# Performance work log

Hardware: AMD Instinct MI355X
Metric: run time of the kernel (lower is better)

## Reference

```python
import jax, jax.numpy as jnp
import numpy as np

N = 50000      # nodes
E = 500000     # edges
D = 128        # model dim (in_dim == out_dim)
H = 8          # heads
DH = D // H    # head dim = 16
BN_EPS = 1e-5
Z_EPS = 1e-6


def setup_inputs() -> dict:
    key = jax.random.key(0)
    ks = jax.random.split(key, 24)
    w = lambda k, shape, s=0.05: (jax.random.normal(k, shape, jnp.float32) * s)
    inp = {}
    inp['v'] = jax.random.normal(ks[0], (N, D), jnp.float32)
    inp['e'] = jax.random.normal(ks[1], (E, D), jnp.float32)
    inp['envelope'] = jax.random.uniform(ks[2], (E, 1, 1), jnp.float32)
    inp['src'] = jax.random.randint(ks[3], (E,), 0, N, jnp.int32)
    inp['dst'] = jax.random.randint(ks[4], (E,), 0, N, jnp.int32)
    # attention projections (use_bias=False)
    inp['WQ'] = w(ks[5], (D, D)); inp['WK'] = w(ks[6], (D, D))
    inp['WV'] = w(ks[7], (D, D)); inp['We'] = w(ks[8], (D, D))
    # output projections
    inp['WO_v'] = w(ks[9], (D, D)); inp['bO_v'] = jnp.zeros((D,), jnp.float32)
    inp['WO_e'] = w(ks[10], (D, D)); inp['bO_e'] = jnp.zeros((D,), jnp.float32)
    # batch-norm affine params
    inp['g1_v'] = jnp.ones((D,), jnp.float32); inp['b1_v'] = jnp.zeros((D,), jnp.float32)
    inp['g1_e'] = jnp.ones((D,), jnp.float32); inp['b1_e'] = jnp.zeros((D,), jnp.float32)
    inp['g2_v'] = jnp.ones((D,), jnp.float32); inp['b2_v'] = jnp.zeros((D,), jnp.float32)
    inp['g2_e'] = jnp.ones((D,), jnp.float32); inp['b2_e'] = jnp.zeros((D,), jnp.float32)
    # FFN weights (hidden = 2*D)
    inp['W1v'] = w(ks[11], (D, 2 * D)); inp['b1v'] = jnp.zeros((2 * D,), jnp.float32)
    inp['W2v'] = w(ks[12], (2 * D, D)); inp['b2v'] = jnp.zeros((D,), jnp.float32)
    inp['W1e'] = w(ks[13], (D, 2 * D)); inp['b1e'] = jnp.zeros((2 * D,), jnp.float32)
    inp['W2e'] = w(ks[14], (2 * D, D)); inp['b2e'] = jnp.zeros((D,), jnp.float32)
    return inp


def _batchnorm(x, g, b):
    # BatchNorm1d in training mode: biased batch stats over axis 0
    m = x.mean(0)
    var = x.var(0)
    return (x - m) * jax.lax.rsqrt(var + BN_EPS) * g + b


def _forward(v, e, envelope, src, dst,
             WQ, WK, WV, We, WO_v, bO_v, WO_e, bO_e,
             g1_v, b1_v, g1_e, b1_e,
             W1v, b1v, W2v, b2v, W1e, b1e, W2e, b2e,
             g2_v, b2_v, g2_e, b2_e):
    # --- multi-head edge attention ---
    Q = (v @ WQ).reshape(N, H, DH)
    K = (v @ WK).reshape(N, H, DH)
    V = (v @ WV).reshape(N, H, DH)
    pe = (e @ We).reshape(E, H, DH)
    # score = K[src] * Q[dst] / sqrt(Dh) * proj_e   (elementwise, per head)
    score = K[src] * Q[dst] / np.sqrt(DH).astype(np.float32) * pe  # [E,H,Dh]
    e_attn = score.reshape(E, D)                                    # e_out
    s = jnp.exp(jnp.clip(score.sum(-1, keepdims=True), -5.0, 5.0))  # [E,H,1]
    msg = V[src] * envelope * s                                     # [E,H,Dh]
    wV = jax.ops.segment_sum(msg, dst, num_segments=N)              # [N,H,Dh]
    z = jax.ops.segment_sum(s, dst, num_segments=N)                 # [N,H,1]
    v_attn = (wV / (z + Z_EPS)).reshape(N, D)
    # --- O projection + residual + batchnorm ---
    v1 = _batchnorm(v + (v_attn @ WO_v + bO_v), g1_v, b1_v)
    e1 = _batchnorm(e + (e_attn @ WO_e + bO_e), g1_e, b1_e)
    # --- FFN + residual + batchnorm ---
    v2 = _batchnorm(v1 + (jax.nn.relu(v1 @ W1v + b1v) @ W2v + b2v), g2_v, b2_v)
    e2 = _batchnorm(e1 + (jax.nn.relu(e1 @ W1e + b1e) @ W2e + b2e), g2_e, b2_e)
    return v2, e2


def reference(v, e, envelope, src, dst,
              WQ, WK, WV, We, WO_v, bO_v, WO_e, bO_e,
              g1_v, b1_v, g1_e, b1_e,
              W1v, b1v, W2v, b2v, W1e, b1e, W2e, b2e,
              g2_v, b2_v, g2_e, b2_e):
    return _forward(v, e, envelope, src, dst,
                    WQ, WK, WV, We, WO_v, bO_v, WO_e, bO_e,
                    g1_v, b1_v, g1_e, b1_e,
                    W1v, b1v, W2v, b2v, W1e, b1e, W2e, b2e,
                    g2_v, b2_v, g2_e, b2_e)
```

## Files before the change

kernel.cpp:

```cpp
#include <hip/hip_runtime.h>
#include <hip/hip_bf16.h>

#define N_NODES 50000
#define N_EDGES 500000
#define DIM 128
#define RSTRIDE 256

typedef __bf16 bf16_t;
typedef __bf16 bf16x8 __attribute__((ext_vector_type(8)));
typedef __bf16 bf16x2 __attribute__((ext_vector_type(2)));
typedef float f32x4 __attribute__((ext_vector_type(4)));

#define MFMA(a,b,c) __builtin_amdgcn_mfma_f32_16x16x32_bf16((a),(b),(c),0,0,0)

__device__ __forceinline__ int swz(int row, int kbyte){ return kbyte ^ ((row & 7) << 4); }
__device__ __forceinline__ int hswz(int row, int kbyte){ return kbyte ^ ((row & 15) << 4); }

__device__ __forceinline__ bf16x8 lds_frag(const char* s, int row, int rowb, int kbyte){
  return *(const bf16x8*)(s + row * rowb + swz(row, kbyte));
}

__device__ __forceinline__ void copy16(char* dst, const char* __restrict__ src, int bytes){
  for (int o = threadIdx.x * 16; o < bytes; o += blockDim.x * 16)
    *(f32x4*)(dst + o) = *(const f32x4*)(src + o);
}

struct WPrep {
  const float* w[10];
  int Kd[10], Nd[10], off[10], cum[10], mode[10];
};

__global__ void k_wprep(WPrep d, char* img, int total){
  for (int idx = blockIdx.x * blockDim.x + threadIdx.x; idx < total; idx += gridDim.x * blockDim.x){
    int i = 0;
#pragma unroll
    for (int j = 1; j < 10; j++) if (idx >= d.cum[j]) i = j;
    int loc = idx - d.cum[i];
    int K = d.Kd[i], N = d.Nd[i];
    int n = loc / K, k = loc - n * K;
    float val = d.w[i][(size_t)k * N + n];
    int nn = n;
    if (d.mode[i] == 1) nn = ((n & 7) << 4) | (n >> 3);
    if (d.mode[i] == 3) nn = ((n & 15) << 4) | (n >> 4);
    *(bf16_t*)(img + d.off[i] + nn * (K * 2) + swz(nn, k * 2)) = (bf16_t)val;
  }
}

__global__ void k_count(const int* __restrict__ dst, int* __restrict__ cnt){
  int i = blockIdx.x * blockDim.x + threadIdx.x;
  if (i < N_EDGES) atomicAdd(&cnt[dst[i]], 1);
}

__global__ __launch_bounds__(1024) void k_scan(const int* __restrict__ cnt,
                                               int* __restrict__ rowptr, int* __restrict__ wp){
  __shared__ int wsum[16];
  __shared__ int wpre[16];
  __shared__ int scarry;
  const int tid = threadIdx.x, lane = tid & 63, wv = tid >> 6;
  if (tid == 0) scarry = 0;
  for (int base = 0; base < N_NODES; base += 8192){
    int i0 = base + tid * 8;
    int v[8], p[8];
    int tsum = 0;
#pragma unroll
    for (int j = 0; j < 8; j++){
      int idx = i0 + j;
      v[j] = (idx < N_NODES) ? cnt[idx] : 0;
      p[j] = tsum; tsum += v[j];
    }
    int x = tsum;
#pragma unroll
    for (int off = 1; off < 64; off <<= 1){
      int t = __shfl_up(x, off);
      if (lane >= off) x += t;
    }
    if (lane == 63) wsum[wv] = x;
    __syncthreads();
    if (tid == 0){
      int run = scarry;
#pragma unroll
      for (int j = 0; j < 16; j++){ int t = wsum[j]; wpre[j] = run; run += t; }
      scarry = run;
    }
    __syncthreads();
    int texcl = wpre[wv] + x - tsum;
#pragma unroll
    for (int j = 0; j < 8; j++){
      int idx = i0 + j;
      if (idx < N_NODES){ rowptr[idx] = texcl + p[j]; wp[idx] = texcl + p[j]; }
    }
  }
  __syncthreads();
  if (tid == 0) rowptr[N_NODES] = scarry;
}

__global__ void k_fill(const int* __restrict__ dst, int* __restrict__ wp, int* __restrict__ csr){
  int i = blockIdx.x * blockDim.x + threadIdx.x;
  if (i < N_EDGES){
    int p = atomicAdd(&wp[dst[i]], 1);
    csr[p] = i;
  }
}

__global__ __launch_bounds__(512) void k_qkv(
    const float* __restrict__ v, const char* __restrict__ img,
    bf16_t* __restrict__ Q, bf16_t* __restrict__ K, bf16_t* __restrict__ V, int M)
{
  __shared__ __align__(16) char sm[65536];
  char* sX = sm;
  char* sW = sm + 32768;
  const int tid = threadIdx.x, lane = tid & 63, wave = tid >> 6;
  const int r0 = blockIdx.x * 128;
  for (int c = tid; c < 2048; c += 512){
    int row = c >> 4, kc = c & 15, grow = r0 + row;
    float f[8];
    if (grow < M){
      const float4* p = (const float4*)(v + (size_t)grow * DIM + kc * 8);
      float4 u0 = p[0], u1 = p[1];
      f[0]=u0.x; f[1]=u0.y; f[2]=u0.z; f[3]=u0.w;
      f[4]=u1.x; f[5]=u1.y; f[6]=u1.z; f[7]=u1.w;
    } else {
#pragma unroll
      for (int j=0;j<8;j++) f[j] = 0.f;
    }
    bf16x8 o;
#pragma unroll
    for (int j=0;j<8;j++) o[j] = (bf16_t)f[j];
    *(bf16x8*)(sX + row * 256 + swz(row, kc * 16)) = o;
  }
  const int rowA = wave * 16 + (lane & 15);
  const int kb0 = (lane >> 4) * 16;
  const int crow = wave*16 + (lane >> 4)*4;
  const int ccol = lane & 15;
  const f32x4 zero4 = {0.f, 0.f, 0.f, 0.f};
#pragma unroll
  for (int w3 = 0; w3 < 3; w3++){
    __syncthreads();
    copy16(sW, img + w3 * 32768, 32768);
    __syncthreads();
    f32x4 acc[8];
#pragma unroll
    for (int b=0;b<8;b++) acc[b] = zero4;
#pragma unroll
    for (int ks=0; ks<4; ks++){
      bf16x8 a = lds_frag(sX, rowA, 256, ks*64 + kb0);
#pragma unroll
      for (int nt=0; nt<8; nt++){
        int rn = nt*16 + (lane & 15);
        bf16x8 b = lds_frag(sW, rn, 256, ks*64 + kb0);
        acc[nt] = MFMA(a, b, acc[nt]);
      }
    }
    bf16_t* o = (w3 == 0) ? Q : ((w3 == 1) ? K : V);
#pragma unroll
    for (int r=0; r<4; r++){
      int grow = r0 + crow + r;
      if (grow < M){
        bf16x8 t;
#pragma unroll
        for (int nt=0; nt<8; nt++) t[nt] = (bf16_t)acc[nt][r];
        *(bf16x8*)(o + (size_t)grow * DIM + ccol*8) = t;
      }
    }
  }
}

__global__ __launch_bounds__(512, 4) void k_edge(
    const float* __restrict__ e,
    const int* __restrict__ src, const int* __restrict__ dst,
    const bf16_t* __restrict__ Qb, const bf16_t* __restrict__ Kb,
    const char* __restrict__ imgWe, const char* __restrict__ imgWo,
    const float* __restrict__ bOe,
    bf16_t* __restrict__ e1_pre, float* __restrict__ sv,
    float* __restrict__ stats, int M)
{
  __shared__ __align__(16) char sm[66560];
  char* sW = sm;
  char* sX = sm + 32768;
  float* sStats = (float*)(sm + 65536);
  const int tid = threadIdx.x, lane = tid & 63, wave = tid >> 6;
  const int r0 = blockIdx.x * 128;
  const int crow = wave*16 + (lane >> 4)*4;
  const int ccol = lane & 15;
  const int rowA = wave * 16 + (lane & 15);
  const int q = lane >> 4;
  const int kb0 = q * 16;
  bf16x8 Kg[4], Qg[4];
#pragma unroll
  for (int r=0;r<4;r++){
    int ed = r0 + crow + r; if (ed >= M) ed = M - 1;
    int sn = src[ed], dn = dst[ed];
    Kg[r] = *(const bf16x8*)(Kb + (size_t)sn * DIM + ccol * 8);
    Qg[r] = *(const bf16x8*)(Qb + (size_t)dn * DIM + ccol * 8);
  }
  int grA = r0 + rowA; if (grA >= M) grA = M - 1;
  const f32x4* epA = (const f32x4*)(e + (size_t)grA * DIM);
  f32x4 ea[8];
#pragma unroll
  for (int ks=0; ks<4; ks++){
    ea[2*ks]   = epA[ks*8 + q*2];
    ea[2*ks+1] = epA[ks*8 + q*2 + 1];
  }
  copy16(sW, imgWe, 32768);
  if (tid < 256) sStats[tid] = 0.f;
  bf16x8 eAb[4];
#pragma unroll
  for (int ks=0; ks<4; ks++){
#pragma unroll
    for (int j=0;j<4;j++){
      eAb[ks][j]   = (bf16_t)ea[2*ks][j];
      eAb[ks][4+j] = (bf16_t)ea[2*ks+1][j];
    }
  }
  __syncthreads();
  const f32x4 zero4 = {0.f,0.f,0.f,0.f};
  f32x4 wbuf[4];
#pragma unroll
  for (int i=0;i<4;i++) wbuf[i] = *(const f32x4*)(imgWo + tid*16 + i*8192);
  f32x4 pe[8];
#pragma unroll
  for (int i=0;i<8;i++) pe[i] = zero4;
#pragma unroll
  for (int ks=0; ks<4; ks++){
#pragma unroll
    for (int nt=0; nt<8; nt++){
      int rn = nt*16 + (lane & 15);
      bf16x8 b = lds_frag(sW, rn, 256, ks*64 + kb0);
      pe[nt] = MFMA(eAb[ks], b, pe[nt]);
    }
  }
  __syncthreads();
#pragma unroll
  for (int i=0;i<4;i++) *(f32x4*)(sW + tid*16 + i*8192) = wbuf[i];
  f32x4 er[8];
#pragma unroll
  for (int r=0;r<4;r++){
    int gr = r0 + crow + r; if (gr >= M) gr = M - 1;
    const f32x4* rp = (const f32x4*)(e + (size_t)gr*DIM + ccol*8);
    er[2*r]   = rp[0];
    er[2*r+1] = rp[1];
  }
#pragma unroll
  for (int r=0;r<4;r++){
    int row = crow + r;
    bf16x8 t;
    float hsum = 0.f;
#pragma unroll
    for (int nt=0; nt<8; nt++){
      float sc = pe[nt][r] * 0.25f * (float)Kg[r][nt] * (float)Qg[r][nt];
      t[nt] = (bf16_t)sc;
      hsum += sc;
    }
    *(bf16x8*)(sX + row*256 + swz(row, ccol*16)) = t;
    float ts = hsum + __shfl_xor(hsum, 1);
    int ed = r0 + row;
    if (!(ccol & 1) && ed < M)
      sv[(size_t)ed*8 + (ccol >> 1)] = __expf(fminf(5.f, fmaxf(-5.f, ts)));
  }
  __syncthreads();
  f32x4 a2[8];
#pragma unroll
  for (int i=0;i<8;i++) a2[i] = zero4;
#pragma unroll
  for (int ks=0; ks<4; ks++){
    bf16x8 a = lds_frag(sX, rowA, 256, ks*64 + kb0);
#pragma unroll
    for (int nt=0; nt<8; nt++){
      int rn = nt*16 + (lane & 15);
      bf16x8 b = lds_frag(sW, rn, 256, ks*64 + kb0);
      a2[nt] = MFMA(a, b, a2[nt]);
    }
  }
  float4 bo0 = *(const float4*)(bOe + ccol*8);
  float4 bo1 = *(const float4*)(bOe + ccol*8 + 4);
  float s1[8], s2[8];
#pragma unroll
  for (int j=0;j<8;j++){ s1[j]=0.f; s2[j]=0.f; }
#pragma unroll
  for (int r=0; r<4; r++){
    int ed = r0 + crow + r;
    float val[8];
    if (ed < M){
      val[0]=a2[0][r]+er[2*r][0]+bo0.x; val[1]=a2[1][r]+er[2*r][1]+bo0.y;
      val[2]=a2[2][r]+er[2*r][2]+bo0.z; val[3]=a2[3][r]+er[2*r][3]+bo0.w;
      val[4]=a2[4][r]+er[2*r+1][0]+bo1.x; val[5]=a2[5][r]+er[2*r+1][1]+bo1.y;
      val[6]=a2[6][r]+er[2*r+1][2]+bo1.z; val[7]=a2[7][r]+er[2*r+1][3]+bo1.w;
      bf16x8 t;
#pragma unroll
      for (int j=0;j<8;j++) t[j] = (bf16_t)val[j];
      *(bf16x8*)(e1_pre + (size_t)ed*RSTRIDE + ccol*8) = t;
    } else {
#pragma unroll
      for (int j=0;j<8;j++) val[j]=0.f;
    }
#pragma unroll
    for (int j=0;j<8;j++){ s1[j] += val[j]; s2[j] += val[j]*val[j]; }
  }
#pragma unroll
  for (int j=0;j<8;j++){
    s1[j] += __shfl_xor(s1[j], 16); s1[j] += __shfl_xor(s1[j], 32);
    s2[j] += __shfl_xor(s2[j], 16); s2[j] += __shfl_xor(s2[j], 32);
  }
  if (lane < 16){
#pragma unroll
    for (int j=0;j<8;j++){
      atomicAdd(&sStats[ccol*8 + j], s1[j]);
      atomicAdd(&sStats[128 + ccol*8 + j], s2[j]);
    }
  }
  __syncthreads();
  if (tid < 256) unsafeAtomicAdd(&stats[tid], sStats[tid]);
}

__global__ __launch_bounds__(512) void k_agg(
    const int* __restrict__ rowptr, const int* __restrict__ csr,
    const int* __restrict__ src, const float* __restrict__ envl,
    const float* __restrict__ sv, const bf16_t* __restrict__ V,
    bf16_t* __restrict__ vAttn, int M)
{
  const int wave = threadIdx.x >> 6, lane = threadIdx.x & 63;
  const int n = blockIdx.x * 8 + wave;
  if (n >= M) return;
  const int beg = rowptr[n], end = rowptr[n + 1];
  const int h = lane >> 3;
  float ax = 0.f, ay = 0.f, zacc = 0.f;
  int i = beg;
  for (; i + 4 <= end; i += 4){
    int e0 = csr[i], e1 = csr[i+1], e2 = csr[i+2], e3 = csr[i+3];
    int sn0 = src[e0], sn1 = src[e1], sn2 = src[e2], sn3 = src[e3];
    float sv0 = sv[(size_t)e0*8 + h], sv1 = sv[(size_t)e1*8 + h];
    float sv2 = sv[(size_t)e2*8 + h], sv3 = sv[(size_t)e3*8 + h];
    float n0 = envl[e0], n1 = envl[e1], n2 = envl[e2], n3 = envl[e3];
    bf16x2 a0 = *(const bf16x2*)(V + (size_t)sn0 * DIM + lane * 2);
    bf16x2 a1 = *(const bf16x2*)(V + (size_t)sn1 * DIM + lane * 2);
    bf16x2 a2v = *(const bf16x2*)(V + (size_t)sn2 * DIM + lane * 2);
    bf16x2 a3 = *(const bf16x2*)(V + (size_t)sn3 * DIM + lane * 2);
    float w0 = n0*sv0, w1 = n1*sv1, w2 = n2*sv2, w3 = n3*sv3;
    ax += (float)a0[0]*w0 + (float)a1[0]*w1 + (float)a2v[0]*w2 + (float)a3[0]*w3;
    ay += (float)a0[1]*w0 + (float)a1[1]*w1 + (float)a2v[1]*w2 + (float)a3[1]*w3;
    zacc += sv0 + sv1 + sv2 + sv3;
// ... 69 lines not shown
      const float4* vp = (const float4*)(v + (size_t)grow*DIM + ccol*8);
      float4 v0 = vp[0], v1 = vp[1];
      val[0]=acc[0][r]+v0.x+bo0.x; val[1]=acc[1][r]+v0.y+bo0.y;
      val[2]=acc[2][r]+v0.z+bo0.z; val[3]=acc[3][r]+v0.w+bo0.w;
      val[4]=acc[4][r]+v1.x+bo1.x; val[5]=acc[5][r]+v1.y+bo1.y;
      val[6]=acc[6][r]+v1.z+bo1.z; val[7]=acc[7][r]+v1.w+bo1.w;
      bf16x8 t;
#pragma unroll
      for (int j=0;j<8;j++) t[j] = (bf16_t)val[j];
      *(bf16x8*)(v1_pre + (size_t)grow*RSTRIDE + ccol*8) = t;
    } else {
#pragma unroll
      for (int j=0;j<8;j++) val[j]=0.f;
    }
#pragma unroll
    for (int j=0;j<8;j++){ s1[j] += val[j]; s2[j] += val[j]*val[j]; }
  }
#pragma unroll
  for (int j=0;j<8;j++){
    s1[j] += __shfl_xor(s1[j], 16); s1[j] += __shfl_xor(s1[j], 32);
    s2[j] += __shfl_xor(s2[j], 16); s2[j] += __shfl_xor(s2[j], 32);
  }
  if (lane < 16){
#pragma unroll
    for (int j=0;j<8;j++){
      atomicAdd(&sStats[ccol*8 + j], s1[j]);
      atomicAdd(&sStats[128 + ccol*8 + j], s2[j]);
    }
  }
  __syncthreads();
  if (tid < 256) unsafeAtomicAdd(&stats[tid], sStats[tid]);
}

__global__ __launch_bounds__(512, 4) void k_ffn(
    bf16_t* __restrict__ xio, const float* __restrict__ ss1,
    const char* __restrict__ img1, const float* __restrict__ b1,
    const char* __restrict__ img2, const float* __restrict__ b2,
    float* __restrict__ stats2, int M)
{
  __shared__ __align__(16) char sm[66560];
  char* sA = sm;
  char* sB = sm + 32768;
  float* sStats = (float*)(sm + 65536);
  const int tid = threadIdx.x, lane = tid & 63, wave = tid >> 6;
  const int r0 = blockIdx.x * 128;
  const int rowA = wave*16 + (lane & 15);
  const int q = lane >> 4;
  const int kb0 = q * 16;
  const int crow = wave*16 + q*4;
  const int ccol = lane & 15;
  const f32x4 zero4 = {0.f,0.f,0.f,0.f};

  float4 sc0 = *(const float4*)(ss1 + ccol*8);
  float4 sc1 = *(const float4*)(ss1 + ccol*8 + 4);
  float4 sh0 = *(const float4*)(ss1 + 128 + ccol*8);
  float4 sh1 = *(const float4*)(ss1 + 128 + ccol*8 + 4);
  const float4* bq = (const float4*)(b1 + ccol * 16);
  float4 bq0 = bq[0], bq1 = bq[1], bq2 = bq[2], bq3 = bq[3];

  copy16(sB, img1, 32768);
  if (tid < 256) sStats[tid] = 0.f;
  int grA = r0 + rowA; if (grA >= M) grA = M - 1;
  const bf16_t* xrow = xio + (size_t)grA * RSTRIDE;
  bf16x8 araw[4];
#pragma unroll
  for (int ks=0; ks<4; ks++)
// ... 88 lines not shown
      t[6]=(bf16_t)fmaxf(acc[6][r]+bq3.z,0.f); t[7]=(bf16_t)fmaxf(acc[7][r]+bq3.w,0.f);
      hreg[4+r] = t;
    }
  }
  __syncthreads();

  f32x4 o2[8];
#pragma unroll
  for (int i=0;i<8;i++) o2[i]=zero4;

#pragma unroll
  for (int half = 0; half < 2; half++){
    if ((ccol >> 3) == half){
      int cb = (ccol & 7) * 32;
#pragma unroll
      for (int r=0;r<4;r++){
        int row = crow + r;
        *(bf16x8*)(sA + row*256 + hswz(row, cb))      = hreg[r];
        *(bf16x8*)(sA + row*256 + hswz(row, cb + 16)) = hreg[4+r];
      }
    }
#pragma unroll
    for (int i=0;i<4;i++) *(f32x4*)(sB + tid*16 + i*8192) = wbuf[i];
    __syncthreads();
    if (half == 0){
#pragma unroll
      for (int i=0;i<4;i++){
        int o = tid*16 + i*8192;
        wbuf[i] = *(const f32x4*)(img2 + (o >> 8)*512 + 256 + (o & 255));
      }
    }
#pragma unroll
    for (int ks=0;ks<4;ks++){
      const char* ap = sA + rowA*256 + hswz(rowA, ks*64+kb0);
      bf16x8 a = *(const bf16x8*)ap;
#pragma unroll
      for (int nt=0;nt<8;nt++){
        int rn = nt*16 + (lane&15);
        bf16x8 b = lds_frag(sB, rn, 256, ks*64+kb0);
        o2[nt] = MFMA(a,b,o2[nt]);
      }
    }
    __syncthreads();
  }

  float4 b20 = *(const float4*)(b2 + ccol*8);
  float4 b21 = *(const float4*)(b2 + ccol*8 + 4);
  float s1[8], s2[8];
#pragma unroll
  for (int j=0;j<8;j++){ s1[j]=0.f; s2[j]=0.f; }
#pragma unroll
  for (int r=0;r<4;r++){
    int grow = r0 + crow + r;
    float val[8];
    val[0]=(float)xres[r][0]+o2[0][r]+b20.x; val[1]=(float)xres[r][1]+o2[1][r]+b20.y;
    val[2]=(float)xres[r][2]+o2[2][r]+b20.z; val[3]=(float)xres[r][3]+o2[3][r]+b20.w;
    val[4]=(float)xres[r][4]+o2[4][r]+b21.x; val[5]=(float)xres[r][5]+o2[5][r]+b21.y;
    val[6]=(float)xres[r][6]+o2[6][r]+b21.z; val[7]=(float)xres[r][7]+o2[7][r]+b21.w;
    if (grow < M){
      bf16x8 t;
#pragma unroll
      for (int j=0;j<8;j++) t[j] = (bf16_t)val[j];
      *(bf16x8*)(xio + (size_t)grow*RSTRIDE + ccol*8) = t;
    } else {
#pragma unroll
      for (int j=0;j<8;j++) val[j]=0.f;
    }
#pragma unroll
    for (int j=0;j<8;j++){ s1[j] += val[j]; s2[j] += val[j]*val[j]; }
  }
#pragma unroll
  for (int j=0;j<8;j++){
    s1[j] += __shfl_xor(s1[j], 16); s1[j] += __shfl_xor(s1[j], 32);
    s2[j] += __shfl_xor(s2[j], 16); s2[j] += __shfl_xor(s2[j], 32);
  }
  if (lane < 16){
#pragma unroll
    for (int j=0;j<8;j++){
      atomicAdd(&sStats[ccol*8 + j], s1[j]);
      atomicAdd(&sStats[128 + ccol*8 + j], s2[j]);
    }
  }
  __syncthreads();
  if (tid < 256) unsafeAtomicAdd(&stats2[tid], sStats[tid]);
}

struct FinArgs { const float* st; const float* g; const float* b; float* ss; float invM; };

__global__ void k_finstats(FinArgs a0, FinArgs a1){
  FinArgs a = (blockIdx.x == 0) ? a0 : a1;
  int c = threadIdx.x;
  float mean = a.st[c] * a.invM;
  float var  = a.st[128 + c] * a.invM - mean * mean;
  float scl  = a.g[c] * rsqrtf(var + 1e-5f);
  a.ss[c] = scl;
  a.ss[128 + c] = a.b[c] - mean * scl;
}

__global__ __launch_bounds__(256) void k_norm2(
    char* __restrict__ xv, char* __restrict__ xe,
    const float* __restrict__ ssv, const float* __restrict__ sse,
    long long nv, long long ne)
{
  long long tv = nv * 16, total = tv + ne * 16;
  for (long long g = (long long)blockIdx.x * blockDim.x + threadIdx.x; g < total;
       g += (long long)gridDim.x * blockDim.x){
    bool isv = g < tv;
    char* base = isv ? xv : xe;
    const float* ss = isv ? ssv : sse;
    long long gg = isv ? g : g - tv;
    long long row = gg >> 4;
    int c = (int)(gg & 15);
    bf16x8 u = *(const bf16x8*)(base + row * 512 + c * 16);
    int c0 = c * 8;
    float4 o0, o1;
    o0.x = (float)u[0]*ss[c0+0] + ss[128+c0+0];
    o0.y = (float)u[1]*ss[c0+1] + ss[128+c0+1];
    o0.z = (float)u[2]*ss[c0+2] + ss[128+c0+2];
    o0.w = (float)u[3]*ss[c0+3] + ss[128+c0+3];
    o1.x = (float)u[4]*ss[c0+4] + ss[128+c0+4];
    o1.y = (float)u[5]*ss[c0+5] + ss[128+c0+5];
    o1.z = (float)u[6]*ss[c0+6] + ss[128+c0+6];
    o1.w = (float)u[7]*ss[c0+7] + ss[128+c0+7];
    float4* dp = (float4*)(base + row * 512 + c * 32);
    dp[0] = o0; dp[1] = o1;
  }
}

extern "C" void kernel_launch(void* const* d_in, const int* in_sizes, int n_in,
                              void* d_out, int out_size, void* d_ws, size_t ws_size,
                              hipStream_t stream)
{
  const float* v    = (const float*)d_in[0];
  const float* e    = (const float*)d_in[1];
  const float* envl = (const float*)d_in[2];
  const int*   src  = (const int*)d_in[3];
  const int*   dst  = (const int*)d_in[4];
  const float* bOv  = (const float*)d_in[10];
  const float* bOe  = (const float*)d_in[12];
  const float* g1v  = (const float*)d_in[13];
  const float* b1vn = (const float*)d_in[14];
  const float* g1e  = (const float*)d_in[15];
// ... 11 lines not shown
  float* out_e = out_v + (size_t)N_NODES * DIM;
  bf16_t* v1b = (bf16_t*)out_v;
  bf16_t* e1b = (bf16_t*)out_e;

  char* ws = (char*)d_ws;
  const size_t IMG_OFF = 0;
  const size_t QB_OFF  = 458752;
  const size_t KB_OFF  = QB_OFF  + 12800000;
  const size_t VB_OFF  = KB_OFF  + 12800000;
  const size_t VA_OFF  = VB_OFF  + 12800000;
  const size_t SV_OFF  = VA_OFF  + 12800000;
  const size_t CSR_OFF = SV_OFF  + 16000000;
  const size_t RP_OFF  = CSR_OFF + 2000000;
  const size_t WP_OFF  = RP_OFF  + 200016;
  const size_t CNT_OFF = WP_OFF  + 200000;
  const size_t ST_OFF  = CNT_OFF + 200000;
  const size_t SS_OFF  = ST_OFF  + 4096;

  char*   img   = ws + IMG_OFF;
  bf16_t* Qb    = (bf16_t*)(ws + QB_OFF);
  bf16_t* Kb    = (bf16_t*)(ws + KB_OFF);
  bf16_t* Vb    = (bf16_t*)(ws + VB_OFF);
  bf16_t* vAttn = (bf16_t*)(ws + VA_OFF);
  float*  svp   = (float*)(ws + SV_OFF);
  int*    csr   = (int*)(ws + CSR_OFF);
  int*    rowp  = (int*)(ws + RP_OFF);
  int*    wpp   = (int*)(ws + WP_OFF);
  int*    cnt   = (int*)(ws + CNT_OFF);
  float*  st    = (float*)(ws + ST_OFF);
  float*  ssb   = (float*)(ws + SS_OFF);
  float* st_e1 = st;        float* st_v1 = st + 256;
  float* st_v2 = st + 512;  float* st_e2 = st + 768;
  float* ss_v1 = ssb;       float* ss_e1 = ssb + 256;
  float* ss_v2 = ssb + 512; float* ss_e2 = ssb + 768;

  (void)hipMemsetAsync(ws + CNT_OFF, 0, 200000 + 4096, stream);

  WPrep wp;
  const int wid[10]   = {5,6,7,8,9,11,21,23,25,27};
  const int Ks[10]    = {128,128,128,128,128,128,128,256,128,256};
  const int Ns[10]    = {128,128,128,128,128,128,256,128,256,128};
  const int modes[10] = {1,1,1,1,1,1,3,1,3,1};
  int cum = 0, off = 0;
  for (int i = 0; i < 10; i++){
    wp.w[i] = (const float*)d_in[wid[i]];
    wp.Kd[i] = Ks[i]; wp.Nd[i] = Ns[i];
    wp.off[i] = off; wp.cum[i] = cum; wp.mode[i] = modes[i];
    off += Ks[i]*Ns[i]*2; cum += Ks[i]*Ns[i];
  }
  k_wprep<<<896, 256, 0, stream>>>(wp, img, cum);

  k_count<<<1954, 256, 0, stream>>>(dst, cnt);
  k_scan<<<1, 1024, 0, stream>>>(cnt, rowp, wpp);
  k_fill<<<1954, 256, 0, stream>>>(dst, wpp, csr);

  k_qkv<<<391, 512, 0, stream>>>(v, img, Qb, Kb, Vb, N_NODES);

  k_edge<<<3907, 512, 0, stream>>>(e, src, dst, Qb, Kb,
                                   img + 98304 , img + 163840 , bOe,
                                   e1b, svp, st_e1, N_EDGES);

  k_agg<<<6250, 512, 0, stream>>>(rowp, csr, src, envl, svp, Vb, vAttn, N_NODES);

  k_nodeout<<<391, 512, 0, stream>>>(vAttn, v, img + 131072 , bOv,
                                     v1b, st_v1, N_NODES);

  {
    FinArgs fv{st_v1, g1v, b1vn, ss_v1, 1.f / N_NODES};
    FinArgs fe{st_e1, g1e, b1en, ss_e1, 1.f / N_EDGES};
    k_finstats<<<2, 128, 0, stream>>>(fv, fe);
  }

  k_ffn<<<391, 512, 0, stream>>>(v1b, ss_v1, img + 196608 , b1vf,
                                 img + 262144 , b2vf, st_v2, N_NODES);
  k_ffn<<<3907, 512, 0, stream>>>(e1b, ss_e1, img + 327680 , b1ef,
                                  img + 393216 , b2ef, st_e2, N_EDGES);

  {
    FinArgs fv{st_v2, g2v, b2vn, ss_v2, 1.f / N_NODES};
    FinArgs fe{st_e2, g2e, b2en, ss_e2, 1.f / N_EDGES};
    k_finstats<<<2, 128, 0, stream>>>(fv, fe);
  }

  k_norm2<<<4096, 256, 0, stream>>>((char*)out_v, (char*)out_e, ss_v2, ss_e2,
                                    (long long)N_NODES, (long long)N_EDGES);
}
```

Baseline: 723.9 us.

## Fuse CSR build kernels into weight-prep, QKV and edge kernels; fold finstats into norm

Merges the weight-prep and degree-count kernels into one launch, runs the prefix scan as an extra block alongside the QKV GEMM, and appends the CSR fill as extra blocks of the edge kernel. The final BN stats finalize is computed per block inside the normalization kernel, which removes one more launch. The goal is fewer kernel launches and letting the small serial stages overlap with bigger work. In exchange, the single scan block now has 512 threads and may become the tail of the QKV launch, and every norm block recomputes the scale and shift.

```diff
diff --git a/kernel.cpp b/kernel.cpp
--- a/kernel.cpp
+++ b/kernel.cpp
@@ -30,151 +30,151 @@
   int Kd[10], Nd[10], off[10], cum[10], mode[10];
 };
 
-__global__ void k_wprep(WPrep d, char* img, int total){
-  for (int idx = blockIdx.x * blockDim.x + threadIdx.x; idx < total; idx += gridDim.x * blockDim.x){
-    int i = 0;
-#pragma unroll
-    for (int j = 1; j < 10; j++) if (idx >= d.cum[j]) i = j;
-    int loc = idx - d.cum[i];
-    int K = d.Kd[i], N = d.Nd[i];
-    int n = loc / K, k = loc - n * K;
-    float val = d.w[i][(size_t)k * N + n];
-    int nn = n;
-    if (d.mode[i] == 1) nn = ((n & 7) << 4) | (n >> 3);
-    if (d.mode[i] == 3) nn = ((n & 15) << 4) | (n >> 4);
-    *(bf16_t*)(img + d.off[i] + nn * (K * 2) + swz(nn, k * 2)) = (bf16_t)val;
-  }
-}
-
-__global__ void k_count(const int* __restrict__ dst, int* __restrict__ cnt){
-  int i = blockIdx.x * blockDim.x + threadIdx.x;
-  if (i < N_EDGES) atomicAdd(&cnt[dst[i]], 1);
-}
-
-__global__ __launch_bounds__(1024) void k_scan(const int* __restrict__ cnt,
-                                               int* __restrict__ rowptr, int* __restrict__ wp){
-  __shared__ int wsum[16];
-  __shared__ int wpre[16];
-  __shared__ int scarry;
-  const int tid = threadIdx.x, lane = tid & 63, wv = tid >> 6;
-  if (tid == 0) scarry = 0;
-  for (int base = 0; base < N_NODES; base += 8192){
-    int i0 = base + tid * 8;
-    int v[8], p[8];
-    int tsum = 0;
-#pragma unroll
-    for (int j = 0; j < 8; j++){
-      int idx = i0 + j;
-      v[j] = (idx < N_NODES) ? cnt[idx] : 0;
-      p[j] = tsum; tsum += v[j];
-    }
-    int x = tsum;
-#pragma unroll
-    for (int off = 1; off < 64; off <<= 1){
-      int t = __shfl_up(x, off);
-      if (lane >= off) x += t;
-    }
-    if (lane == 63) wsum[wv] = x;
-    __syncthreads();
-    if (tid == 0){
-      int run = scarry;
-#pragma unroll
-      for (int j = 0; j < 16; j++){ int t = wsum[j]; wpre[j] = run; run += t; }
-      scarry = run;
-    }
-    __syncthreads();
-    int texcl = wpre[wv] + x - tsum;
-#pragma unroll
-    for (int j = 0; j < 8; j++){
-      int idx = i0 + j;
-      if (idx < N_NODES){ rowptr[idx] = texcl + p[j]; wp[idx] = texcl + p[j]; }
-    }
-  }
-  __syncthreads();
-  if (tid == 0) rowptr[N_NODES] = scarry;
-}
-
-__global__ void k_fill(const int* __restrict__ dst, int* __restrict__ wp, int* __restrict__ csr){
-  int i = blockIdx.x * blockDim.x + threadIdx.x;
-  if (i < N_EDGES){
-    int p = atomicAdd(&wp[dst[i]], 1);
-    csr[p] = i;
-  }
-}
-
-__global__ __launch_bounds__(512) void k_qkv(
+__global__ __launch_bounds__(512) void k_prep(WPrep d, char* img,
+                                              const int* __restrict__ dst, int* __restrict__ cnt){
+  if (blockIdx.x < 448){
+    int idx = blockIdx.x * 512 + threadIdx.x;
+    if (idx < 229376){
+      int i = 0;
+#pragma unroll
+      for (int j = 1; j < 10; j++) if (idx >= d.cum[j]) i = j;
+      int loc = idx - d.cum[i];
+      int K = d.Kd[i], N = d.Nd[i];
+      int n = loc / K, k = loc - n * K;
+      float val = d.w[i][(size_t)k * N + n];
+      int nn = n;
+      if (d.mode[i] == 1) nn = ((n & 7) << 4) | (n >> 3);
+      if (d.mode[i] == 3) nn = ((n & 15) << 4) | (n >> 4);
+      *(bf16_t*)(img + d.off[i] + nn * (K * 2) + swz(nn, k * 2)) = (bf16_t)val;
+    }
+  } else {
+    int i = (blockIdx.x - 448) * 512 + threadIdx.x;
+    if (i < N_EDGES) atomicAdd(&cnt[dst[i]], 1);
+  }
+}
+
+__global__ __launch_bounds__(512) void k_qkv_scan(
     const float* __restrict__ v, const char* __restrict__ img,
-    bf16_t* __restrict__ Q, bf16_t* __restrict__ K, bf16_t* __restrict__ V, int M)
+    bf16_t* __restrict__ Q, bf16_t* __restrict__ K, bf16_t* __restrict__ V, int M,
+    const int* __restrict__ cnt, int* __restrict__ rowptr, int* __restrict__ wp)
 {
   __shared__ __align__(16) char sm[65536];
-  char* sX = sm;
-  char* sW = sm + 32768;
+  __shared__ int wsum[8], wpre[8], scarry_s;
   const int tid = threadIdx.x, lane = tid & 63, wave = tid >> 6;
-  const int r0 = blockIdx.x * 128;
-  for (int c = tid; c < 2048; c += 512){
-    int row = c >> 4, kc = c & 15, grow = r0 + row;
-    float f[8];
-    if (grow < M){
-      const float4* p = (const float4*)(v + (size_t)grow * DIM + kc * 8);
-      float4 u0 = p[0], u1 = p[1];
-      f[0]=u0.x; f[1]=u0.y; f[2]=u0.z; f[3]=u0.w;
-      f[4]=u1.x; f[5]=u1.y; f[6]=u1.z; f[7]=u1.w;
-    } else {
-#pragma unroll
-      for (int j=0;j<8;j++) f[j] = 0.f;
-    }
-    bf16x8 o;
-#pragma unroll
-    for (int j=0;j<8;j++) o[j] = (bf16_t)f[j];
-    *(bf16x8*)(sX + row * 256 + swz(row, kc * 16)) = o;
-  }
-  const int rowA = wave * 16 + (lane & 15);
-  const int kb0 = (lane >> 4) * 16;
-  const int crow = wave*16 + (lane >> 4)*4;
-  const int ccol = lane & 15;
-  const f32x4 zero4 = {0.f, 0.f, 0.f, 0.f};
-#pragma unroll
-  for (int w3 = 0; w3 < 3; w3++){
-    __syncthreads();
-    copy16(sW, img + w3 * 32768, 32768);
-    __syncthreads();
-    f32x4 acc[8];
-#pragma unroll
-    for (int b=0;b<8;b++) acc[b] = zero4;
-#pragma unroll
-    for (int ks=0; ks<4; ks++){
-      bf16x8 a = lds_frag(sX, rowA, 256, ks*64 + kb0);
-#pragma unroll
-      for (int nt=0; nt<8; nt++){
-        int rn = nt*16 + (lane & 15);
-        bf16x8 b = lds_frag(sW, rn, 256, ks*64 + kb0);
-        acc[nt] = MFMA(a, b, acc[nt]);
-      }
-    }
-    bf16_t* o = (w3 == 0) ? Q : ((w3 == 1) ? K : V);
-#pragma unroll
-    for (int r=0; r<4; r++){
-      int grow = r0 + crow + r;
+  if (blockIdx.x < 391){
+    char* sX = sm;
+    char* sW = sm + 32768;
+    const int r0 = blockIdx.x * 128;
+    for (int c = tid; c < 2048; c += 512){
+      int row = c >> 4, kc = c & 15, grow = r0 + row;
+      float f[8];
       if (grow < M){
-        bf16x8 t;
-#pragma unroll
-        for (int nt=0; nt<8; nt++) t[nt] = (bf16_t)acc[nt][r];
-        *(bf16x8*)(o + (size_t)grow * DIM + ccol*8) = t;
-      }
-    }
-  }
-}
-
-__global__ __launch_bounds__(512, 4) void k_edge(
+        const float4* p = (const float4*)(v + (size_t)grow * DIM + kc * 8);
+        float4 u0 = p[0], u1 = p[1];
+        f[0]=u0.x; f[1]=u0.y; f[2]=u0.z; f[3]=u0.w;
+        f[4]=u1.x; f[5]=u1.y; f[6]=u1.z; f[7]=u1.w;
+      } else {
+#pragma unroll
+        for (int j=0;j<8;j++) f[j] = 0.f;
+      }
+      bf16x8 o;
+#pragma unroll
+      for (int j=0;j<8;j++) o[j] = (bf16_t)f[j];
+      *(bf16x8*)(sX + row * 256 + swz(row, kc * 16)) = o;
+    }
+    const int rowA = wave * 16 + (lane & 15);
+    const int kb0 = (lane >> 4) * 16;
+    const int crow = wave*16 + (lane >> 4)*4;
+    const int ccol = lane & 15;
+    const f32x4 zero4 = {0.f, 0.f, 0.f, 0.f};
+#pragma unroll
+    for (int w3 = 0; w3 < 3; w3++){
+      __syncthreads();
+      copy16(sW, img + w3 * 32768, 32768);
+      __syncthreads();
+      f32x4 acc[8];
+#pragma unroll
+      for (int b=0;b<8;b++) acc[b] = zero4;
+#pragma unroll
+      for (int ks=0; ks<4; ks++){
+        bf16x8 a = lds_frag(sX, rowA, 256, ks*64 + kb0);
+#pragma unroll
+        for (int nt=0; nt<8; nt++){
+          int rn = nt*16 + (lane & 15);
+          bf16x8 b = lds_frag(sW, rn, 256, ks*64 + kb0);
+          acc[nt] = MFMA(a, b, acc[nt]);
+        }
+      }
+      bf16_t* o = (w3 == 0) ? Q : ((w3 == 1) ? K : V);
+#pragma unroll
+      for (int r=0; r<4; r++){
+        int grow = r0 + crow + r;
+        if (grow < M){
+          bf16x8 t;
+#pragma unroll
+          for (int nt=0; nt<8; nt++) t[nt] = (bf16_t)acc[nt][r];
+          *(bf16x8*)(o + (size_t)grow * DIM + ccol*8) = t;
+        }
+      }
+    }
+  } else {
+    if (tid == 0) scarry_s = 0;
+    for (int base = 0; base < N_NODES; base += 4096){
+      int i0 = base + tid * 8;
+      int vv[8], pp[8];
+      int tsum = 0;
+#pragma unroll
+      for (int j = 0; j < 8; j++){
+        int idx = i0 + j;
+        vv[j] = (idx < N_NODES) ? cnt[idx] : 0;
+        pp[j] = tsum; tsum += vv[j];
+      }
+      int x = tsum;
+#pragma unroll
+      for (int off = 1; off < 64; off <<= 1){
+        int t = __shfl_up(x, off);
+        if (lane >= off) x += t;
+      }
+      if (lane == 63) wsum[wave] = x;
+      __syncthreads();
+      if (tid == 0){
+        int run = scarry_s;
+#pragma unroll
+        for (int j = 0; j < 8; j++){ int t = wsum[j]; wpre[j] = run; run += t; }
+        scarry_s = run;
+      }
+      __syncthreads();
+      int texcl = wpre[wave] + x - tsum;
+#pragma unroll
+      for (int j = 0; j < 8; j++){
+        int idx = i0 + j;
+        if (idx < N_NODES){ rowptr[idx] = texcl + pp[j]; wp[idx] = texcl + pp[j]; }
+      }
+      __syncthreads();
+    }
+    if (tid == 0) rowptr[N_NODES] = scarry_s;
+  }
+}
+
+__global__ __launch_bounds__(512, 4) void k_edge_fill(
     const float* __restrict__ e,
     const int* __restrict__ src, const int* __restrict__ dst,
     const bf16_t* __restrict__ Qb, const bf16_t* __restrict__ Kb,
     const char* __restrict__ imgWe, const char* __restrict__ imgWo,
     const float* __restrict__ bOe,
     bf16_t* __restrict__ e1_pre, float* __restrict__ sv,
-    float* __restrict__ stats, int M)
+    float* __restrict__ stats, int M,
+    int* __restrict__ wpF, int* __restrict__ csrF)
 {
   __shared__ __align__(16) char sm[66560];
+  if (blockIdx.x >= 3907){
+    int i = (blockIdx.x - 3907) * 512 + threadIdx.x;
+    if (i < N_EDGES){
+      int pp = atomicAdd(&wpF[dst[i]], 1);
+      csrF[pp] = i;
+    }
+    return;
+  }
   char* sW = sm;
   char* sX = sm + 32768;
   float* sStats = (float*)(sm + 65536);
@@ -441,6 +441,18 @@
   if (tid < 256) unsafeAtomicAdd(&stats[tid], sStats[tid]);
 }
 
+struct FinArgs { const float* st; const float* g; const float* b; float* ss; float invM; };
+
+__global__ void k_finstats(FinArgs a0, FinArgs a1){
+  FinArgs a = (blockIdx.x == 0) ? a0 : a1;
+  int c = threadIdx.x;
+  float mean = a.st[c] * a.invM;
+  float var  = a.st[128 + c] * a.invM - mean * mean;
+  float scl  = a.g[c] * rsqrtf(var + 1e-5f);
+  a.ss[c] = scl;
+  a.ss[128 + c] = a.b[c] - mean * scl;
+}
+
 __global__ __launch_bounds__(512, 4) void k_ffn(
     bf16_t* __restrict__ xio, const float* __restrict__ ss1,
     const char* __restrict__ img1, const float* __restrict__ b1,
@@ -595,8 +607,7 @@
     }
 #pragma unroll
     for (int ks=0;ks<4;ks++){
-      const char* ap = sA + rowA*256 + hswz(rowA, ks*64+kb0);
-      bf16x8 a = *(const bf16x8*)ap;
+      bf16x8 a = *(const bf16x8*)(sA + rowA*256 + hswz(rowA, ks*64+kb0));
 #pragma unroll
       for (int nt=0;nt<8;nt++){
         int rn = nt*16 + (lane&15);
@@ -648,29 +659,30 @@
   if (tid < 256) unsafeAtomicAdd(&stats2[tid], sStats[tid]);
 }
 
-struct FinArgs { const float* st; const float* g; const float* b; float* ss; float invM; };
-
-__global__ void k_finstats(FinArgs a0, FinArgs a1){
-  FinArgs a = (blockIdx.x == 0) ? a0 : a1;
-  int c = threadIdx.x;
-  float mean = a.st[c] * a.invM;
-  float var  = a.st[128 + c] * a.invM - mean * mean;
-  float scl  = a.g[c] * rsqrtf(var + 1e-5f);
-  a.ss[c] = scl;
-  a.ss[128 + c] = a.b[c] - mean * scl;
-}
+struct NormP { const float* st; const float* g; const float* bn; float invM; };
 
 __global__ __launch_bounds__(256) void k_norm2(
     char* __restrict__ xv, char* __restrict__ xe,
-    const float* __restrict__ ssv, const float* __restrict__ sse,
-    long long nv, long long ne)
+    NormP pv, NormP pe, long long nv, long long ne)
 {
+  __shared__ float sSS[512];
+  const int tid = threadIdx.x;
+  {
+    int side = tid >> 7, c = tid & 127;
+    NormP pp = side ? pe : pv;
+    float mean = pp.st[c] * pp.invM;
+    float var  = pp.st[128 + c] * pp.invM - mean * mean;
+    float scl  = pp.g[c] * rsqrtf(var + 1e-5f);
+    sSS[side*256 + c] = scl;
+    sSS[side*256 + 128 + c] = pp.bn[c] - mean * scl;
+  }
+  __syncthreads();
   long long tv = nv * 16, total = tv + ne * 16;
-  for (long long g = (long long)blockIdx.x * blockDim.x + threadIdx.x; g < total;
+  for (long long g = (long long)blockIdx.x * blockDim.x + tid; g < total;
        g += (long long)gridDim.x * blockDim.x){
     bool isv = g < tv;
     char* base = isv ? xv : xe;
-    const float* ss = isv ? ssv : sse;
+    const float* ss = isv ? sSS : (sSS + 256);
     long long gg = isv ? g : g - tv;
     long long row = gg >> 4;
     int c = (int)(gg & 15);
@@ -748,7 +760,6 @@
   float* st_e1 = st;        float* st_v1 = st + 256;
   float* st_v2 = st + 512;  float* st_e2 = st + 768;
   float* ss_v1 = ssb;       float* ss_e1 = ssb + 256;
-  float* ss_v2 = ssb + 512; float* ss_e2 = ssb + 768;
 
   (void)hipMemsetAsync(ws + CNT_OFF, 0, 200000 + 4096, stream);
 
@@ -764,40 +775,26 @@
     wp.off[i] = off; wp.cum[i] = cum; wp.mode[i] = modes[i];
     off += Ks[i]*Ns[i]*2; cum += Ks[i]*Ns[i];
   }
-  k_wprep<<<896, 256, 0, stream>>>(wp, img, cum);
-
-  k_count<<<1954, 256, 0, stream>>>(dst, cnt);
-  k_scan<<<1, 1024, 0, stream>>>(cnt, rowp, wpp);
-  k_fill<<<1954, 256, 0, stream>>>(dst, wpp, csr);
-
-  k_qkv<<<391, 512, 0, stream>>>(v, img, Qb, Kb, Vb, N_NODES);
-
-  k_edge<<<3907, 512, 0, stream>>>(e, src, dst, Qb, Kb,
-                                   img + 98304 , img + 163840 , bOe,
-                                   e1b, svp, st_e1, N_EDGES);
-
+
+  k_prep<<<1425, 512, 0, stream>>>(wp, img, dst, cnt);
+  k_qkv_scan<<<392, 512, 0, stream>>>(v, img, Qb, Kb, Vb, N_NODES, cnt, rowp, wpp);
+  k_edge_fill<<<4884, 512, 0, stream>>>(e, src, dst, Qb, Kb,
+                                        img + 98304 , img + 163840 , bOe,
+                                        e1b, svp, st_e1, N_EDGES, wpp, csr);
   k_agg<<<6250, 512, 0, stream>>>(rowp, csr, src, envl, svp, Vb, vAttn, N_NODES);
-
   k_nodeout<<<391, 512, 0, stream>>>(vAttn, v, img + 131072 , bOv,
                                      v1b, st_v1, N_NODES);
-
   {
     FinArgs fv{st_v1, g1v, b1vn, ss_v1, 1.f / N_NODES};
     FinArgs fe{st_e1, g1e, b1en, ss_e1, 1.f / N_EDGES};
     k_finstats<<<2, 128, 0, stream>>>(fv, fe);
   }
-
   k_ffn<<<391, 512, 0, stream>>>(v1b, ss_v1, img + 196608 , b1vf,
                                  img + 262144 , b2vf, st_v2, N_NODES);
   k_ffn<<<3907, 512, 0, stream>>>(e1b, ss_e1, img + 327680 , b1ef,
                                   img + 393216 , b2ef, st_e2, N_EDGES);
-
-  {
-    FinArgs fv{st_v2, g2v, b2vn, ss_v2, 1.f / N_NODES};
-    FinArgs fe{st_e2, g2e, b2en, ss_e2, 1.f / N_EDGES};
-    k_finstats<<<2, 128, 0, stream>>>(fv, fe);
-  }
-
-  k_norm2<<<4096, 256, 0, stream>>>((char*)out_v, (char*)out_e, ss_v2, ss_e2,
+  NormP npv{st_v2, g2v, b2vn, 1.f / N_NODES};
+  NormP npe{st_e2, g2e, b2en, 1.f / N_EDGES};
+  k_norm2<<<4096, 256, 0, stream>>>((char*)out_v, (char*)out_e, npv, npe,
                                     (long long)N_NODES, (long long)N_EDGES);
 }
```

After: 749.9 us. 1.04x slower.

## Halve k_edge LDS by transposing O-projection and fold final BN stats into norm

Applied to the files above, without the earlier changes.

The edge kernel's second GEMM now keeps the WO_e weight fragments in registers as the A operand (using a transposed weight image) and reads the score tile from LDS as B. This lets one 32KB buffer serve both weights and scores, halving LDS so more blocks can be resident. The epilogue is rewritten for the transposed accumulator layout, with per-column shuffles and direct stats stores instead of LDS atomics. The final k_finstats launch is removed by computing scale/shift inside k_norm2 per block, which adds redundant small work in every block. The residual e is reloaded with narrower, less coalesced accesses, and a __syncthreads is moved inside the scan loop.

```diff
diff --git a/kernel.cpp b/kernel.cpp
--- a/kernel.cpp
+++ b/kernel.cpp
@@ -8,6 +8,7 @@
 
 typedef __bf16 bf16_t;
 typedef __bf16 bf16x8 __attribute__((ext_vector_type(8)));
+typedef __bf16 bf16x4 __attribute__((ext_vector_type(4)));
 typedef __bf16 bf16x2 __attribute__((ext_vector_type(2)));
 typedef float f32x4 __attribute__((ext_vector_type(4)));
 
@@ -89,8 +90,8 @@
       int idx = i0 + j;
       if (idx < N_NODES){ rowptr[idx] = texcl + p[j]; wp[idx] = texcl + p[j]; }
     }
-  }
-  __syncthreads();
+    __syncthreads();
+  }
   if (tid == 0) rowptr[N_NODES] = scarry;
 }
 
@@ -174,16 +175,14 @@
     bf16_t* __restrict__ e1_pre, float* __restrict__ sv,
     float* __restrict__ stats, int M)
 {
-  __shared__ __align__(16) char sm[66560];
-  char* sW = sm;
-  char* sX = sm + 32768;
-  float* sStats = (float*)(sm + 65536);
+  __shared__ __align__(16) char sm[33792];
+  char* sBuf = sm;
+  float* sStats = (float*)(sm + 32768);
   const int tid = threadIdx.x, lane = tid & 63, wave = tid >> 6;
   const int r0 = blockIdx.x * 128;
-  const int crow = wave*16 + (lane >> 4)*4;
-  const int ccol = lane & 15;
-  const int rowA = wave * 16 + (lane & 15);
-  const int q = lane >> 4;
+  const int q = lane >> 4, ccol = lane & 15;
+  const int crow = wave*16 + q*4;
+  const int rowA = wave*16 + ccol;
   const int kb0 = q * 16;
   bf16x8 Kg[4], Qg[4];
 #pragma unroll
@@ -201,8 +200,7 @@
     ea[2*ks]   = epA[ks*8 + q*2];
     ea[2*ks+1] = epA[ks*8 + q*2 + 1];
   }
-  copy16(sW, imgWe, 32768);
-  if (tid < 256) sStats[tid] = 0.f;
+  copy16(sBuf, imgWe, 32768);
   bf16x8 eAb[4];
 #pragma unroll
   for (int ks=0; ks<4; ks++){
@@ -214,9 +212,6 @@
   }
   __syncthreads();
   const f32x4 zero4 = {0.f,0.f,0.f,0.f};
-  f32x4 wbuf[4];
-#pragma unroll
-  for (int i=0;i<4;i++) wbuf[i] = *(const f32x4*)(imgWo + tid*16 + i*8192);
   f32x4 pe[8];
 #pragma unroll
   for (int i=0;i<8;i++) pe[i] = zero4;
@@ -224,22 +219,11 @@
   for (int ks=0; ks<4; ks++){
 #pragma unroll
     for (int nt=0; nt<8; nt++){
-      int rn = nt*16 + (lane & 15);
-      bf16x8 b = lds_frag(sW, rn, 256, ks*64 + kb0);
+      bf16x8 b = lds_frag(sBuf, nt*16 + ccol, 256, ks*64 + kb0);
       pe[nt] = MFMA(eAb[ks], b, pe[nt]);
     }
   }
   __syncthreads();
-#pragma unroll
-  for (int i=0;i<4;i++) *(f32x4*)(sW + tid*16 + i*8192) = wbuf[i];
-  f32x4 er[8];
-#pragma unroll
-  for (int r=0;r<4;r++){
-    int gr = r0 + crow + r; if (gr >= M) gr = M - 1;
-    const f32x4* rp = (const f32x4*)(e + (size_t)gr*DIM + ccol*8);
-    er[2*r]   = rp[0];
-    er[2*r+1] = rp[1];
-  }
 #pragma unroll
   for (int r=0;r<4;r++){
     int row = crow + r;
@@ -251,61 +235,64 @@
       t[nt] = (bf16_t)sc;
       hsum += sc;
     }
-    *(bf16x8*)(sX + row*256 + swz(row, ccol*16)) = t;
+    *(bf16x8*)(sBuf + row*256 + swz(row, ccol*16)) = t;
     float ts = hsum + __shfl_xor(hsum, 1);
     int ed = r0 + row;
     if (!(ccol & 1) && ed < M)
       sv[(size_t)ed*8 + (ccol >> 1)] = __expf(fminf(5.f, fmaxf(-5.f, ts)));
   }
+  bf16x8 w2a[4];
+#pragma unroll
+  for (int ks=0; ks<4; ks++)
+    w2a[ks] = *(const bf16x8*)(imgWo + rowA*256 + swz(rowA, ks*64 + kb0));
   __syncthreads();
   f32x4 a2[8];
 #pragma unroll
   for (int i=0;i<8;i++) a2[i] = zero4;
 #pragma unroll
   for (int ks=0; ks<4; ks++){
-    bf16x8 a = lds_frag(sX, rowA, 256, ks*64 + kb0);
 #pragma unroll
     for (int nt=0; nt<8; nt++){
-      int rn = nt*16 + (lane & 15);
-      bf16x8 b = lds_frag(sW, rn, 256, ks*64 + kb0);
-      a2[nt] = MFMA(a, b, a2[nt]);
-    }
-  }
-  float4 bo0 = *(const float4*)(bOe + ccol*8);
-  float4 bo1 = *(const float4*)(bOe + ccol*8 + 4);
-  float s1[8], s2[8];
-#pragma unroll
-  for (int j=0;j<8;j++){ s1[j]=0.f; s2[j]=0.f; }
-#pragma unroll
-  for (int r=0; r<4; r++){
-    int ed = r0 + crow + r;
-    float val[8];
-    if (ed < M){
-      val[0]=a2[0][r]+er[2*r][0]+bo0.x; val[1]=a2[1][r]+er[2*r][1]+bo0.y;
-      val[2]=a2[2][r]+er[2*r][2]+bo0.z; val[3]=a2[3][r]+er[2*r][3]+bo0.w;
-      val[4]=a2[4][r]+er[2*r+1][0]+bo1.x; val[5]=a2[5][r]+er[2*r+1][1]+bo1.y;
-      val[6]=a2[6][r]+er[2*r+1][2]+bo1.z; val[7]=a2[7][r]+er[2*r+1][3]+bo1.w;
-      bf16x8 t;
-#pragma unroll
-      for (int j=0;j<8;j++) t[j] = (bf16_t)val[j];
-      *(bf16x8*)(e1_pre + (size_t)ed*RSTRIDE + ccol*8) = t;
+      bf16x8 b = lds_frag(sBuf, nt*16 + ccol, 256, ks*64 + kb0);
+      a2[nt] = MFMA(w2a[ks], b, a2[nt]);
+    }
+  }
+  float4 bo = *(const float4*)(bOe + crow);
+  float s1[4] = {0.f,0.f,0.f,0.f}, s2[4] = {0.f,0.f,0.f,0.f};
+#pragma unroll
+  for (int nt=0; nt<8; nt++){
+    int erow = r0 + nt*16 + ccol;
+    int gr = (erow < M) ? erow : (M - 1);
+    f32x4 er = *(const f32x4*)(e + (size_t)gr*DIM + crow);
+    float val[4];
+    val[0] = a2[nt][0] + er[0] + bo.x;
+    val[1] = a2[nt][1] + er[1] + bo.y;
+    val[2] = a2[nt][2] + er[2] + bo.z;
+    val[3] = a2[nt][3] + er[3] + bo.w;
+    if (erow < M){
+      bf16x4 t;
+#pragma unroll
+      for (int r=0;r<4;r++) t[r] = (bf16_t)val[r];
+      *(bf16x4*)(e1_pre + (size_t)erow*RSTRIDE + crow) = t;
     } else {
 #pragma unroll
-      for (int j=0;j<8;j++) val[j]=0.f;
-    }
-#pragma unroll
-    for (int j=0;j<8;j++){ s1[j] += val[j]; s2[j] += val[j]*val[j]; }
-  }
-#pragma unroll
-  for (int j=0;j<8;j++){
-    s1[j] += __shfl_xor(s1[j], 16); s1[j] += __shfl_xor(s1[j], 32);
-    s2[j] += __shfl_xor(s2[j], 16); s2[j] += __shfl_xor(s2[j], 32);
-  }
-  if (lane < 16){
-#pragma unroll
-    for (int j=0;j<8;j++){
-      atomicAdd(&sStats[ccol*8 + j], s1[j]);
-      atomicAdd(&sStats[128 + ccol*8 + j], s2[j]);
+      for (int r=0;r<4;r++) val[r] = 0.f;
+    }
+#pragma unroll
+    for (int r=0;r<4;r++){ s1[r] += val[r]; s2[r] += val[r]*val[r]; }
+  }
+#pragma unroll
+  for (int r=0;r<4;r++){
+    s1[r] += __shfl_xor(s1[r], 1); s1[r] += __shfl_xor(s1[r], 2);
+    s1[r] += __shfl_xor(s1[r], 4); s1[r] += __shfl_xor(s1[r], 8);
+    s2[r] += __shfl_xor(s2[r], 1); s2[r] += __shfl_xor(s2[r], 2);
+    s2[r] += __shfl_xor(s2[r], 4); s2[r] += __shfl_xor(s2[r], 8);
+  }
+  if (ccol == 0){
+#pragma unroll
+    for (int r=0;r<4;r++){
+      sStats[crow + r] = s1[r];
+      sStats[128 + crow + r] = s2[r];
     }
   }
   __syncthreads();
@@ -441,6 +428,18 @@
   if (tid < 256) unsafeAtomicAdd(&stats[tid], sStats[tid]);
 }
 
+struct FinArgs { const float* st; const float* g; const float* b; float* ss; float invM; };
+
+__global__ void k_finstats(FinArgs a0, FinArgs a1){
+  FinArgs a = (blockIdx.x == 0) ? a0 : a1;
+  int c = threadIdx.x;
+  float mean = a.st[c] * a.invM;
+  float var  = a.st[128 + c] * a.invM - mean * mean;
+  float scl  = a.g[c] * rsqrtf(var + 1e-5f);
+  a.ss[c] = scl;
+  a.ss[128 + c] = a.b[c] - mean * scl;
+}
+
 __global__ __launch_bounds__(512, 4) void k_ffn(
     bf16_t* __restrict__ xio, const float* __restrict__ ss1,
     const char* __restrict__ img1, const float* __restrict__ b1,
@@ -595,8 +594,7 @@
     }
 #pragma unroll
     for (int ks=0;ks<4;ks++){
-      const char* ap = sA + rowA*256 + hswz(rowA, ks*64+kb0);
-      bf16x8 a = *(const bf16x8*)ap;
+      bf16x8 a = *(const bf16x8*)(sA + rowA*256 + hswz(rowA, ks*64+kb0));
 #pragma unroll
       for (int nt=0;nt<8;nt++){
         int rn = nt*16 + (lane&15);
@@ -648,29 +646,30 @@
   if (tid < 256) unsafeAtomicAdd(&stats2[tid], sStats[tid]);
 }
 
-struct FinArgs { const float* st; const float* g; const float* b; float* ss; float invM; };
-
-__global__ void k_finstats(FinArgs a0, FinArgs a1){
-  FinArgs a = (blockIdx.x == 0) ? a0 : a1;
-  int c = threadIdx.x;
-  float mean = a.st[c] * a.invM;
-  float var  = a.st[128 + c] * a.invM - mean * mean;
-  float scl  = a.g[c] * rsqrtf(var + 1e-5f);
-  a.ss[c] = scl;
-  a.ss[128 + c] = a.b[c] - mean * scl;
-}
+struct NormP { const float* st; const float* g; const float* bn; float invM; };
 
 __global__ __launch_bounds__(256) void k_norm2(
     char* __restrict__ xv, char* __restrict__ xe,
-    const float* __restrict__ ssv, const float* __restrict__ sse,
-    long long nv, long long ne)
+    NormP pv, NormP pe, long long nv, long long ne)
 {
+  __shared__ float sSS[512];
+  const int tid = threadIdx.x;
+  {
+    int side = tid >> 7, c = tid & 127;
+    NormP pp = side ? pe : pv;
+    float mean = pp.st[c] * pp.invM;
+    float var  = pp.st[128 + c] * pp.invM - mean * mean;
+    float scl  = pp.g[c] * rsqrtf(var + 1e-5f);
+    sSS[side*256 + c] = scl;
+    sSS[side*256 + 128 + c] = pp.bn[c] - mean * scl;
+  }
+  __syncthreads();
   long long tv = nv * 16, total = tv + ne * 16;
-  for (long long g = (long long)blockIdx.x * blockDim.x + threadIdx.x; g < total;
+  for (long long g = (long long)blockIdx.x * blockDim.x + tid; g < total;
        g += (long long)gridDim.x * blockDim.x){
     bool isv = g < tv;
     char* base = isv ? xv : xe;
-    const float* ss = isv ? ssv : sse;
+    const float* ss = isv ? sSS : (sSS + 256);
     long long gg = isv ? g : g - tv;
     long long row = gg >> 4;
     int c = (int)(gg & 15);
@@ -748,7 +747,6 @@
   float* st_e1 = st;        float* st_v1 = st + 256;
   float* st_v2 = st + 512;  float* st_e2 = st + 768;
   float* ss_v1 = ssb;       float* ss_e1 = ssb + 256;
-  float* ss_v2 = ssb + 512; float* ss_e2 = ssb + 768;
 
   (void)hipMemsetAsync(ws + CNT_OFF, 0, 200000 + 4096, stream);
 
@@ -756,7 +754,7 @@
   const int wid[10]   = {5,6,7,8,9,11,21,23,25,27};
   const int Ks[10]    = {128,128,128,128,128,128,128,256,128,256};
   const int Ns[10]    = {128,128,128,128,128,128,256,128,256,128};
-  const int modes[10] = {1,1,1,1,1,1,3,1,3,1};
+  const int modes[10] = {1,1,1,1,1,0,3,1,3,1};
   int cum = 0, off = 0;
   for (int i = 0; i < 10; i++){
     wp.w[i] = (const float*)d_in[wid[i]];
@@ -792,12 +790,8 @@
   k_ffn<<<3907, 512, 0, stream>>>(e1b, ss_e1, img + 327680 , b1ef,
                                   img + 393216 , b2ef, st_e2, N_EDGES);
 
-  {
-    FinArgs fv{st_v2, g2v, b2vn, ss_v2, 1.f / N_NODES};
-    FinArgs fe{st_e2, g2e, b2en, ss_e2, 1.f / N_EDGES};
-    k_finstats<<<2, 128, 0, stream>>>(fv, fe);
-  }
-
-  k_norm2<<<4096, 256, 0, stream>>>((char*)out_v, (char*)out_e, ss_v2, ss_e2,
+  NormP npv{st_v2, g2v, b2vn, 1.f / N_NODES};
+  NormP npe{st_e2, g2e, b2en, 1.f / N_EDGES};
+  k_norm2<<<4096, 256, 0, stream>>>((char*)out_v, (char*)out_e, npv, npe,
                                     (long long)N_NODES, (long long)N_EDGES);
 }
```

Measured after the change: 712.0 us. Within noise of the previous version (-1.6%).
